# Kernel optimization log

Measured on AMD Instinct MI355X. Metric: run time of the kernel, lower is better.

Reference implementation:

```python
import jax, jax.numpy as jnp
import numpy as np

N_NODES = 50000
N_EDGES = 800000
IN_DIM = 128
HID = 128
NUM_LAYERS = 3
LN_EPS = 1e-5


def setup_inputs() -> dict:
    key = jax.random.key(0)
    ks = jax.random.split(key, 4 + 4 * NUM_LAYERS)
    x = jax.random.normal(ks[0], (N_NODES, IN_DIM), dtype=jnp.float32)
    edge_index = jax.random.randint(ks[1], (2, N_EDGES), 0, N_NODES, dtype=jnp.int32)
    Ws, bs, gammas, betas = [], [], [], []
    d_in = IN_DIM
    for l in range(NUM_LAYERS):
        scale = 1.0 / np.sqrt(d_in)
        Ws.append(jax.random.uniform(ks[2 + 4 * l], (d_in, HID), jnp.float32, -scale, scale))
        bs.append(jnp.zeros((HID,), jnp.float32))
        gammas.append(jnp.ones((HID,), jnp.float32))
        betas.append(jnp.zeros((HID,), jnp.float32))
        d_in = HID
    return {"x": x, "edge_index": edge_index, "Ws": Ws, "bs": bs,
            "gammas": gammas, "betas": betas}


def _gcn_conv(x, src, dst, dinv, norm_e, W, b):
    # GCNConv: h = x W; out = D^{-1/2}(A+I)D^{-1/2} h + b (self loops added)
    h = x @ W                                        # [N, H]
    msg = h[src] * norm_e[:, None]                   # [E, H] gather
    agg = jax.ops.segment_sum(msg, dst, num_segments=N_NODES)  # scatter
    agg = agg + h * (dinv * dinv)[:, None]           # self-loop contribution
    return agg + b


def _layernorm(x, gamma, beta):
    mu = jnp.mean(x, axis=-1, keepdims=True)
    var = jnp.mean(jnp.square(x - mu), axis=-1, keepdims=True)
    return (x - mu) * jax.lax.rsqrt(var + LN_EPS) * gamma + beta


def reference(x, edge_index, Ws, bs, gammas, betas):
    src, dst = edge_index[0], edge_index[1]
    # degree with self loops (PyG: counts on target index, +1 for self loop)
    deg = jax.ops.segment_sum(jnp.ones((N_EDGES,), x.dtype), dst,
                              num_segments=N_NODES) + 1.0
    dinv = jax.lax.rsqrt(deg)                        # deg >= 1 always
    norm_e = dinv[src] * dinv[dst]                   # [E]
    emb = x
    for i in range(NUM_LAYERS):
        h = _gcn_conv(x, src, dst, dinv, norm_e, Ws[i], bs[i])
        emb = h
        x = jax.nn.relu(h)
        # dropout is identity in eval mode
        if i != NUM_LAYERS - 1:
            x = _layernorm(x, gammas[i], betas[i])
    return emb, x
```

## Files before the change

### kernel.cpp

```cpp
#include <hip/hip_runtime.h>
#include <cstddef>

#define HID 128
#define LN_EPS 1e-5f
#define GROWS 8
#define WTP 144

typedef unsigned int uint32;
typedef __attribute__((ext_vector_type(8))) short short8;
typedef __attribute__((ext_vector_type(4))) float f32x4;

__device__ __forceinline__ float wave_sum(float v) {
#pragma unroll
  for (int o = 32; o > 0; o >>= 1) v += __shfl_xor(v, o, 64);
  return v;
}

__device__ __forceinline__ uint32 bf16_rne(float x) {
  uint32 u = __float_as_uint(x);
  u += 0x7fffu + ((u >> 16) & 1u);
  return u >> 16;
}

__device__ __forceinline__ uint32 pack_bf2(float x, float y) {
  uint32 ux = __float_as_uint(x);
  uint32 uy = __float_as_uint(y);
  ux += 0x7fffu + ((ux >> 16) & 1u);
  uy += 0x7fffu + ((uy >> 16) & 1u);
  return (ux >> 16) | (uy & 0xffff0000u);
}

extern "C" __global__ void k_zero(int* __restrict__ p, int n) {
  int i = blockIdx.x * blockDim.x + threadIdx.x;
  if (i < n) p[i] = 0;
}

extern "C" __global__ void k_deg(const int* __restrict__ dst, int* __restrict__ deg, int E) {
  int i = blockIdx.x * blockDim.x + threadIdx.x;
  if (i < E) atomicAdd(&deg[dst[i]], 1);
}

extern "C" __global__ void k_dinv(const int* __restrict__ deg, float* __restrict__ dinv, int N) {
  int i = blockIdx.x * blockDim.x + threadIdx.x;
  if (i < N) dinv[i] = rsqrtf((float)deg[i] + 1.0f);
}

extern "C" __global__ void k_scan1(const int* __restrict__ in, int* __restrict__ exc,
                                   int* __restrict__ bsum, int n) {
  __shared__ int sh[256];
  int tid = threadIdx.x;
  int i = blockIdx.x * 256 + tid;
  int v = (i < n) ? in[i] : 0;
  sh[tid] = v;
  __syncthreads();
  for (int o = 1; o < 256; o <<= 1) {
    int t = (tid >= o) ? sh[tid - o] : 0;
    __syncthreads();
    sh[tid] += t;
    __syncthreads();
  }
  if (i < n) exc[i] = sh[tid] - v;
  if (tid == 255) bsum[blockIdx.x] = sh[255];
}

extern "C" __global__ void k_scan2(const int* __restrict__ bsum, int* __restrict__ bbase, int nb) {
  __shared__ int sh[256];
  int tid = threadIdx.x;
  int v = (tid < nb) ? bsum[tid] : 0;
  sh[tid] = v;
  __syncthreads();
  for (int o = 1; o < 256; o <<= 1) {
    int t = (tid >= o) ? sh[tid - o] : 0;
    __syncthreads();
    sh[tid] += t;
    __syncthreads();
  }
  if (tid < nb) bbase[tid] = sh[tid] - v;
}

extern "C" __global__ void k_scan3(const int* __restrict__ exc, const int* __restrict__ bbase,
                                   const int* __restrict__ deg, int* __restrict__ roff,
                                   int* __restrict__ cursor, float* __restrict__ dinv,
                                   int N, int E) {
  int i = blockIdx.x * blockDim.x + threadIdx.x;
  if (i < N) {
    int o = exc[i] + bbase[i >> 8];
    roff[i] = o;
    cursor[i] = o;
    dinv[i] = rsqrtf((float)deg[i] + 1.0f);
  } else if (i == N) {
    roff[N] = E;
  }
}

extern "C" __global__ void k_fill_p(const int* __restrict__ src, const int* __restrict__ dst,
                                    int* __restrict__ cursor, int* __restrict__ csrc,
                                    int E, int N) {
  int part = blockIdx.x & 7;
  int grp = blockIdx.x >> 3;
  int ngrp = gridDim.x >> 3;
  int lo = (int)((long long)N * part >> 3);
  int hi = (int)((long long)N * (part + 1) >> 3);
  for (int i = grp * blockDim.x + threadIdx.x; i < E; i += ngrp * blockDim.x) {
    int d = dst[i];
    if (d >= lo && d < hi) {
      int pos = atomicAdd(&cursor[d], 1);
      csrc[pos] = src[i];
    }
  }
}

extern "C" __global__ void k_wt3(const float* __restrict__ W0, const float* __restrict__ W1,
                                 const float* __restrict__ W2, unsigned short* __restrict__ wt) {
  int i = blockIdx.x * 256 + threadIdx.x;
  if (i < 3 * HID * HID) {
    int l = i >> 14, r = i & 16383;
    int n = r >> 7, k = r & 127;
    const float* W = (l == 0) ? W0 : ((l == 1) ? W1 : W2);
    wt[i] = (unsigned short)bf16_rne(W[k * HID + n]);
  }
}

template <bool BF>
__global__ __launch_bounds__(256) void k_gemm_t(
    const void* __restrict__ xin, const unsigned short* __restrict__ wt,
    const float* __restrict__ dinv, uint32* __restrict__ gb, int N) {
  __shared__ unsigned short Wt[HID * WTP];
  __shared__ float dv_s[64];
  int tid = threadIdx.x, lane = tid & 63, wv = tid >> 6;
  int r0 = blockIdx.x * 64;
  int nr = min(64, N - r0);
  for (int i = tid; i < 2048; i += 256) {
    short8 v = *(const short8*)(wt + i * 8);
    int n = i >> 4, k0 = (i & 15) * 8;
    *(short8*)&Wt[n * WTP + k0] = v;
  }
  if (tid < 64) dv_s[tid] = (tid < nr) ? dinv[r0 + min(tid, nr - 1)] : 0.f;
  int arow = r0 + wv * 16 + (lane & 15);
  int arow_c = min(arow, N - 1);
  int kb = (lane >> 4) * 8;
  short8 a[4];
  if (BF) {
    const uint32* x32 = (const uint32*)xin;
    const uint32* rp = x32 + (size_t)arow_c * 64 + (kb >> 1);
#pragma unroll
    for (int q = 0; q < 4; ++q) a[q] = *(const short8*)(rp + q * 16);
  } else {
    const float* xf = (const float*)xin;
    const float* rp = xf + (size_t)arow_c * HID + kb;
#pragma unroll
    for (int q = 0; q < 4; ++q) {
      float4 f0 = *(const float4*)(rp + q * 32);
      float4 f1 = *(const float4*)(rp + q * 32 + 4);
      short8 t;
      t[0] = (short)bf16_rne(f0.x);
      t[1] = (short)bf16_rne(f0.y);
      t[2] = (short)bf16_rne(f0.z);
      t[3] = (short)bf16_rne(f0.w);
      t[4] = (short)bf16_rne(f1.x);
      t[5] = (short)bf16_rne(f1.y);
      t[6] = (short)bf16_rne(f1.z);
      t[7] = (short)bf16_rne(f1.w);
      a[q] = t;
    }
  }
  __syncthreads();
  int bn = lane & 15;
#pragma unroll
  for (int c = 0; c < 8; ++c) {
    const unsigned short* wr = &Wt[(c * 16 + bn) * WTP + kb];
    f32x4 acc = {0.f, 0.f, 0.f, 0.f};
    short8 b0 = *(const short8*)(wr + 0);
    short8 b1 = *(const short8*)(wr + 32);
    short8 b2 = *(const short8*)(wr + 64);
    short8 b3 = *(const short8*)(wr + 96);
    acc = __builtin_amdgcn_mfma_f32_16x16x32_bf16(a[0], b0, acc, 0, 0, 0);
    acc = __builtin_amdgcn_mfma_f32_16x16x32_bf16(a[1], b1, acc, 0, 0, 0);
    acc = __builtin_amdgcn_mfma_f32_16x16x32_bf16(a[2], b2, acc, 0, 0, 0);
    acc = __builtin_amdgcn_mfma_f32_16x16x32_bf16(a[3], b3, acc, 0, 0, 0);
#pragma unroll
    for (int reg = 0; reg < 4; ++reg) {
      float v = acc[reg];
      float p = __shfl_xor(v, 1, 64);
      int row = wv * 16 + (lane >> 4) * 4 + reg;
      if (!(lane & 1) && row < nr) {
        float dvv = dv_s[row];
        gb[(size_t)(r0 + row) * 64 + (c * 8 + (bn >> 1))] = pack_bf2(v * dvv, p * dvv);
      }
    }
  }
}

extern "C" __global__ __launch_bounds__(256) void k_agg_bf(
    const uint32* __restrict__ gb, const int* __restrict__ roff, const int* __restrict__ csrc,
    const float* __restrict__ dinv, const float* __restrict__ bias,
    const float* __restrict__ gamma, const float* __restrict__ beta,
    uint32* __restrict__ out_bf, float* __restrict__ out0, float* __restrict__ out1,
    int N, int mode) {
  int w = (int)((blockIdx.x * blockDim.x + threadIdx.x) >> 6);
  int lane = threadIdx.x & 63;
  if (w >= N) return;
  uint32 us = gb[(size_t)w * 64 + lane];
  int e = roff[w], e1 = roff[w + 1];
  float ax = __uint_as_float(us << 16);
  float ay = __uint_as_float(us & 0xffff0000u);
  for (; e + 8 <= e1; e += 8) {
#pragma unroll
    for (int i = 0; i < 8; ++i) {
      int s = csrc[e + i];
      uint32 u = gb[(size_t)s * 64 + lane];
      ax += __uint_as_float(u << 16);
      ay += __uint_as_float(u & 0xffff0000u);
    }
  }
  if (e < e1) {
#pragma unroll
    for (int i = 0; i < 8; ++i) {
      int idx = e + i;
      int cl = (idx < e1) ? idx : (e1 - 1);
      int s = csrc[cl];
      uint32 u = gb[(size_t)s * 64 + lane];
      float m = (idx < e1) ? 1.f : 0.f;
      ax = fmaf(m, __uint_as_float(u << 16), ax);
      ay = fmaf(m, __uint_as_float(u & 0xffff0000u), ay);
    }
  }
  float dv = dinv[w];
  float2 bb = *(const float2*)(bias + 2 * lane);
  float hx = fmaf(ax, dv, bb.x);
  float hy = fmaf(ay, dv, bb.y);
  if (mode) {
    *(float2*)(out0 + (size_t)w * HID + 2 * lane) = make_float2(hx, hy);
    *(float2*)(out1 + (size_t)w * HID + 2 * lane) =
        make_float2(fmaxf(hx, 0.f), fmaxf(hy, 0.f));
  } else {
    float rx = fmaxf(hx, 0.f), ry = fmaxf(hy, 0.f);
    float mu = wave_sum(rx + ry) * (1.f / HID);
    float dx = rx - mu, dy = ry - mu;
    float var = wave_sum(dx * dx + dy * dy) * (1.f / HID);
    float sc = rsqrtf(var + LN_EPS);
    float2 ga = *(const float2*)(gamma + 2 * lane);
    float2 be = *(const float2*)(beta + 2 * lane);
    out_bf[(size_t)w * 64 + lane] =
        pack_bf2(fmaf(dx * sc, ga.x, be.x), fmaf(dy * sc, ga.y, be.y));
  }
}

extern "C" __global__ __launch_bounds__(256) void k_gemm(
    const float* __restrict__ x, const float* __restrict__ W,
    const float* __restrict__ dinv, float* __restrict__ g, int N) {
  __shared__ float Wl[HID * HID];
  __shared__ float xl[4][GROWS * HID];
  int tid = threadIdx.x;
#pragma unroll
  for (int i = 0; i < (HID * HID / 4) / 256; ++i)
    ((float4*)Wl)[tid + 256 * i] = ((const float4*)W)[tid + 256 * i];
  __syncthreads();
  int wid = tid >> 6, lane = tid & 63;
  float* xw = xl[wid];
  int nchunks = (N + GROWS - 1) / GROWS;
  int gw = blockIdx.x * 4 + wid;
  int nw = gridDim.x * 4;
  for (int chunk = gw; chunk < nchunks; chunk += nw) {
    int r0 = chunk * GROWS;
    int nr = min(GROWS, N - r0);
    const float4* xs = (const float4*)(x + (size_t)r0 * HID);
    float4* xd = (float4*)xw;
    if (nr == GROWS) {
#pragma unroll
      for (int i = 0; i < 4; ++i) xd[lane + 64 * i] = xs[lane + 64 * i];
    } else {
      for (int i = lane; i < nr * (HID / 4); i += 64) xd[i] = xs[i];
    }
    float2 acc[GROWS];
#pragma unroll
    for (int r = 0; r < GROWS; ++r) acc[r] = make_float2(0.f, 0.f);
    for (int k = 0; k < HID; k += 4) {
      float2 w0 = *(const float2*)&Wl[(k + 0) * HID + 2 * lane];
      float2 w1 = *(const float2*)&Wl[(k + 1) * HID + 2 * lane];
      float2 w2 = *(const float2*)&Wl[(k + 2) * HID + 2 * lane];
      float2 w3 = *(const float2*)&Wl[(k + 3) * HID + 2 * lane];
#pragma unroll
      for (int r = 0; r < GROWS; ++r) {
        float4 xq = *(const float4*)&xw[r * HID + k];
        acc[r].x = fmaf(xq.w, w3.x, fmaf(xq.z, w2.x, fmaf(xq.y, w1.x, fmaf(xq.x, w0.x, acc[r].x))));
        acc[r].y = fmaf(xq.w, w3.y, fmaf(xq.z, w2.y, fmaf(xq.y, w1.y, fmaf(xq.x, w0.y, acc[r].y))));
      }
    }
#pragma unroll
    for (int r = 0; r < GROWS; ++r) {
      if (r < nr) {
        float dv = dinv[r0 + r];
        *(float2*)(g + (size_t)(r0 + r) * HID + 2 * lane) =
            make_float2(acc[r].x * dv, acc[r].y * dv);
      }
    }
  }
}

extern "C" __global__ void k_copy(const float* __restrict__ in, float* __restrict__ out, int n4) {
  int i = blockIdx.x * blockDim.x + threadIdx.x;
  if (i < n4) ((float4*)out)[i] = ((const float4*)in)[i];
}

extern "C" __global__ void k_scatter(const float* __restrict__ g, const int* __restrict__ src,
                                     const int* __restrict__ dst, float* __restrict__ acc, int E) {
  int e = (int)((blockIdx.x * blockDim.x + threadIdx.x) >> 6);
  int lane = threadIdx.x & 63;
  if (e >= E) return;
  int s = src[e], d = dst[e];
  float2 v = *(const float2*)(g + (size_t)s * HID + 2 * lane);
  float* p = acc + (size_t)d * HID + 2 * lane;
  atomicAdd(p, v.x);
  atomicAdd(p + 1, v.y);
}

extern "C" __global__ __launch_bounds__(256) void k_fin(
    float* __restrict__ a, const float* __restrict__ dinv, const float* __restrict__ bias,
    const float* __restrict__ gamma, const float* __restrict__ beta, int N, int last) {
  int w = (int)((blockIdx.x * blockDim.x + threadIdx.x) >> 6);
  int lane = threadIdx.x & 63;
  if (w >= N) return;
  float2 acc = *(const float2*)(a + (size_t)w * HID + 2 * lane);
  float dv = dinv[w];
  float2 bb = *(const float2*)(bias + 2 * lane);
  float hx = fmaf(acc.x, dv, bb.x);
  float hy = fmaf(acc.y, dv, bb.y);
  if (last) {
    *(float2*)(a + (size_t)w * HID + 2 * lane) = make_float2(hx, hy);
  } else {
    float rx = fmaxf(hx, 0.f), ry = fmaxf(hy, 0.f);
    float mu = wave_sum(rx + ry) * (1.f / HID);
    float dx = rx - mu, dy = ry - mu;
    float var = wave_sum(dx * dx + dy * dy) * (1.f / HID);
    float sc = rsqrtf(var + LN_EPS);
    float2 ga = *(const float2*)(gamma + 2 * lane);
    float2 be = *(const float2*)(beta + 2 * lane);
    *(float2*)(a + (size_t)w * HID + 2 * lane) =
        make_float2(fmaf(dx * sc, ga.x, be.x), fmaf(dy * sc, ga.y, be.y));
  }
}

extern "C" __global__ void k_relu(const float* __restrict__ in, float* __restrict__ out, int n4) {
  int i = blockIdx.x * blockDim.x + threadIdx.x;
  if (i < n4) {
    float4 v = ((const float4*)in)[i];
    v.x = fmaxf(v.x, 0.f);
    v.y = fmaxf(v.y, 0.f);
    v.z = fmaxf(v.z, 0.f);
    v.w = fmaxf(v.w, 0.f);
    ((float4*)out)[i] = v;
  }
}

extern "C" void kernel_launch(void* const* d_in, const int* in_sizes, int n_in,
                              void* d_out, int out_size, void* d_ws, size_t ws_size,
                              hipStream_t stream) {
  const float* x0 = (const float*)d_in[0];
  const int* ei = (const int*)d_in[1];
  int N = in_sizes[0] / HID;
  int E = in_sizes[1] / 2;

  const float* W[3];
  const float* b[3];
  const float* gm[3];
  const float* bt[3];
  if (n_in >= 14 && in_sizes[2] == HID * HID) {
    for (int l = 0; l < 3; ++l) {
      W[l] = (const float*)d_in[2 + l];
      b[l] = (const float*)d_in[5 + l];
      gm[l] = (const float*)d_in[8 + l];
      bt[l] = (const float*)d_in[11 + l];
    }
  } else if (n_in >= 6) {
    const float* Wc = (const float*)d_in[2];
    const float* bc = (const float*)d_in[3];
    const float* gc = (const float*)d_in[4];
    const float* tc = (const float*)d_in[5];
    for (int l = 0; l < 3; ++l) {
      W[l] = Wc + (size_t)l * HID * HID;
      b[l] = bc + (size_t)l * HID;
      gm[l] = gc + (size_t)l * HID;
      bt[l] = tc + (size_t)l * HID;
    }
  } else {
    return;
  }
  const int* src = ei;
  const int* dst = ei + E;

  float* OUT0 = (float*)d_out;
  float* OUT1 = OUT0 + (size_t)N * HID;

  auto align256 = [](size_t bytes) { return (bytes + 255) & ~(size_t)255; };
  size_t o_dinv = 0;
  size_t o_roff = o_dinv + align256((size_t)N * 4);
  size_t o_csrc = o_roff + align256((size_t)(N + 1) * 4);
  size_t o_wt3 = o_csrc + align256((size_t)E * 4);
  size_t o_gbf = o_wt3 + align256((size_t)3 * HID * HID * 2);
  size_t o_act = o_gbf + align256((size_t)N * 256);
  size_t need_full = o_act + (size_t)N * 256;
  size_t need_scatter = align256((size_t)N * 4);
  if (ws_size < need_scatter) return;

  char* wp = (char*)d_ws;
  float* dinv = (float*)(wp + o_dinv);

  int n4 = N * HID / 4;
  int aggBlocks = (N * 64 + 255) / 256;

  if (ws_size >= need_full) {
    int* roff = (int*)(wp + o_roff);
    int* csrc = (int*)(wp + o_csrc);
    unsigned short* wt3 = (unsigned short*)(wp + o_wt3);
    uint32* gbf = (uint32*)(wp + o_gbf);
    uint32* act = (uint32*)(wp + o_act);

    int* deg = (int*)OUT1;
    int* exc = deg + N;
    int* cursor = exc + N;
    int* bsum = cursor + N;
    int* bbase = bsum + 256;

    k_zero<<<(N + 255) / 256, 256, 0, stream>>>(deg, N);
    k_deg<<<(E + 255) / 256, 256, 0, stream>>>(dst, deg, E);
    int nb = (N + 255) / 256;
    k_scan1<<<nb, 256, 0, stream>>>(deg, exc, bsum, N);
    k_scan2<<<1, 256, 0, stream>>>(bsum, bbase, nb);
    k_scan3<<<(N + 256) / 256, 256, 0, stream>>>(exc, bbase, deg, roff, cursor, dinv, N, E);
    k_fill_p<<<2048, 256, 0, stream>>>(src, dst, cursor, csrc, E, N);
    k_wt3<<<(3 * HID * HID + 255) / 256, 256, 0, stream>>>(W[0], W[1], W[2], wt3);

    int gemmBlocks = (N + 63) / 64;
    k_gemm_t<false><<<gemmBlocks, 256, 0, stream>>>(x0, wt3, dinv, gbf, N);
    k_agg_bf<<<aggBlocks, 256, 0, stream>>>(gbf, roff, csrc, dinv, b[0], gm[0], bt[0],
                                            act, nullptr, nullptr, N, 0);
    k_gemm_t<true><<<gemmBlocks, 256, 0, stream>>>(act, wt3 + HID * HID, dinv, gbf, N);
    k_agg_bf<<<aggBlocks, 256, 0, stream>>>(gbf, roff, csrc, dinv, b[1], gm[1], bt[1],
                                            act, nullptr, nullptr, N, 0);
    k_gemm_t<true><<<gemmBlocks, 256, 0, stream>>>(act, wt3 + 2 * HID * HID, dinv, gbf, N);
    k_agg_bf<<<aggBlocks, 256, 0, stream>>>(gbf, roff, csrc, dinv, b[2], gm[2], bt[2],
                                            nullptr, OUT0, OUT1, N, 3);
  } else {
    int* deg = (int*)OUT1;
    k_zero<<<(N + 255) / 256, 256, 0, stream>>>(deg, N);
    k_deg<<<(E + 255) / 256, 256, 0, stream>>>(dst, deg, E);
    k_dinv<<<(N + 255) / 256, 256, 0, stream>>>(deg, dinv, N);
    int scatBlocks = (E * 64 + 255) / 256;
    for (int l = 0; l < 3; ++l) {
      const float* xin = (l == 0) ? x0 : OUT0;
      int last = (l == 2);
      k_gemm<<<512, 256, 0, stream>>>(xin, W[l], dinv, OUT1, N);
      k_copy<<<(n4 + 255) / 256, 256, 0, stream>>>(OUT1, OUT0, n4);
      k_scatter<<<scatBlocks, 256, 0, stream>>>(OUT1, src, dst, OUT0, E);
      k_fin<<<aggBlocks, 256, 0, stream>>>(OUT0, dinv, b[l], gm[l], bt[l], N, last);
    }
    k_relu<<<(n4 + 255) / 256, 256, 0, stream>>>(OUT0, OUT1, n4);
  }
}
```

Measured before the change: 235.0 us.

## Gather four edges per wave with 16-byte loads in aggregation; fuse setup kernels

The aggregation kernel now splits each wave into four 16-lane groups. Each group handles a different neighbor edge and loads a full 256-byte bf16 row as uint4 per lane, and the partial sums are then reduced across groups with shuffles. The intent is fewer, wider memory transactions and more gathers in flight per wave, at the cost of more registers and extra shuffles. Separately, the degree-zeroing and weight-transpose kernels are merged into one launch to save a kernel launch.

```diff
diff --git a/kernel.cpp b/kernel.cpp
--- a/kernel.cpp
+++ b/kernel.cpp
@@ -30,9 +30,22 @@
   return (ux >> 16) | (uy & 0xffff0000u);
 }
 
-extern "C" __global__ void k_zero(int* __restrict__ p, int n) {
-  int i = blockIdx.x * blockDim.x + threadIdx.x;
-  if (i < n) p[i] = 0;
+extern "C" __global__ void k_setup(int* __restrict__ deg, int N, int zb,
+                                   const float* __restrict__ W0, const float* __restrict__ W1,
+                                   const float* __restrict__ W2, unsigned short* __restrict__ wt) {
+  int bx = blockIdx.x;
+  if (bx < zb) {
+    int i = bx * 256 + threadIdx.x;
+    if (i < N) deg[i] = 0;
+  } else {
+    int i = (bx - zb) * 256 + threadIdx.x;
+    if (i < 3 * HID * HID) {
+      int l = i >> 14, r = i & 16383;
+      int n = r >> 7, k = r & 127;
+      const float* W = (l == 0) ? W0 : ((l == 1) ? W1 : W2);
+      wt[i] = (unsigned short)bf16_rne(W[k * HID + n]);
+    }
+  }
 }
 
 extern "C" __global__ void k_deg(const int* __restrict__ dst, int* __restrict__ deg, int E) {
@@ -110,17 +123,6 @@
   }
 }
 
-extern "C" __global__ void k_wt3(const float* __restrict__ W0, const float* __restrict__ W1,
-                                 const float* __restrict__ W2, unsigned short* __restrict__ wt) {
-  int i = blockIdx.x * 256 + threadIdx.x;
-  if (i < 3 * HID * HID) {
-    int l = i >> 14, r = i & 16383;
-    int n = r >> 7, k = r & 127;
-    const float* W = (l == 0) ? W0 : ((l == 1) ? W1 : W2);
-    wt[i] = (unsigned short)bf16_rne(W[k * HID + n]);
-  }
-}
-
 template <bool BF>
 __global__ __launch_bounds__(256) void k_gemm_t(
     const void* __restrict__ xin, const unsigned short* __restrict__ wt,
@@ -200,49 +202,99 @@
   int w = (int)((blockIdx.x * blockDim.x + threadIdx.x) >> 6);
   int lane = threadIdx.x & 63;
   if (w >= N) return;
-  uint32 us = gb[(size_t)w * 64 + lane];
+  int g = lane >> 4, c = lane & 15;
+  float acc[8];
+  {
+    uint4 u = ((const uint4*)(gb + (size_t)w * 64))[c];
+    float m = (g == 0) ? 1.f : 0.f;
+    acc[0] = m * __uint_as_float(u.x << 16);
+    acc[1] = m * __uint_as_float(u.x & 0xffff0000u);
+    acc[2] = m * __uint_as_float(u.y << 16);
+    acc[3] = m * __uint_as_float(u.y & 0xffff0000u);
+    acc[4] = m * __uint_as_float(u.z << 16);
+    acc[5] = m * __uint_as_float(u.z & 0xffff0000u);
+    acc[6] = m * __uint_as_float(u.w << 16);
+    acc[7] = m * __uint_as_float(u.w & 0xffff0000u);
+  }
   int e = roff[w], e1 = roff[w + 1];
-  float ax = __uint_as_float(us << 16);
-  float ay = __uint_as_float(us & 0xffff0000u);
-  for (; e + 8 <= e1; e += 8) {
+  for (; e + 4 <= e1; e += 4) {
+    int s = csrc[e + g];
+    uint4 u = ((const uint4*)(gb + (size_t)s * 64))[c];
+    acc[0] += __uint_as_float(u.x << 16);
+    acc[1] += __uint_as_float(u.x & 0xffff0000u);
+    acc[2] += __uint_as_float(u.y << 16);
+    acc[3] += __uint_as_float(u.y & 0xffff0000u);
+    acc[4] += __uint_as_float(u.z << 16);
+    acc[5] += __uint_as_float(u.z & 0xffff0000u);
+    acc[6] += __uint_as_float(u.w << 16);
+    acc[7] += __uint_as_float(u.w & 0xffff0000u);
+  }
+  if (g < e1 - e) {
+    int s = csrc[e + g];
+    uint4 u = ((const uint4*)(gb + (size_t)s * 64))[c];
+    acc[0] += __uint_as_float(u.x << 16);
+    acc[1] += __uint_as_float(u.x & 0xffff0000u);
+    acc[2] += __uint_as_float(u.y << 16);
+    acc[3] += __uint_as_float(u.y & 0xffff0000u);
+    acc[4] += __uint_as_float(u.z << 16);
+    acc[5] += __uint_as_float(u.z & 0xffff0000u);
+    acc[6] += __uint_as_float(u.w << 16);
+    acc[7] += __uint_as_float(u.w & 0xffff0000u);
+  }
+#pragma unroll
+  for (int i = 0; i < 8; ++i) {
+    acc[i] += __shfl_xor(acc[i], 16, 64);
+    acc[i] += __shfl_xor(acc[i], 32, 64);
+  }
+  float dv = dinv[w];
+  float4 bb0 = *(const float4*)(bias + c * 8);
+  float4 bb1 = *(const float4*)(bias + c * 8 + 4);
+  float h[8];
+  h[0] = fmaf(acc[0], dv, bb0.x);
+  h[1] = fmaf(acc[1], dv, bb0.y);
+  h[2] = fmaf(acc[2], dv, bb0.z);
+  h[3] = fmaf(acc[3], dv, bb0.w);
+  h[4] = fmaf(acc[4], dv, bb1.x);
+  h[5] = fmaf(acc[5], dv, bb1.y);
+  h[6] = fmaf(acc[6], dv, bb1.z);
+  h[7] = fmaf(acc[7], dv, bb1.w);
+  if (mode) {
+    if (g == 0) {
+      float4* o0 = (float4*)(out0 + (size_t)w * HID + c * 8);
+      o0[0] = make_float4(h[0], h[1], h[2], h[3]);
+      o0[1] = make_float4(h[4], h[5], h[6], h[7]);
+      float4* o1 = (float4*)(out1 + (size_t)w * HID + c * 8);
+      o1[0] = make_float4(fmaxf(h[0], 0.f), fmaxf(h[1], 0.f), fmaxf(h[2], 0.f), fmaxf(h[3], 0.f));
+      o1[1] = make_float4(fmaxf(h[4], 0.f), fmaxf(h[5], 0.f), fmaxf(h[6], 0.f), fmaxf(h[7], 0.f));
+    }
+  } else {
+    float r[8], s8 = 0.f;
 #pragma unroll
     for (int i = 0; i < 8; ++i) {
-      int s = csrc[e + i];
-      uint32 u = gb[(size_t)s * 64 + lane];
-      ax += __uint_as_float(u << 16);
-      ay += __uint_as_float(u & 0xffff0000u);
-    }
-  }
-  if (e < e1) {
+      r[i] = fmaxf(h[i], 0.f);
+      s8 += r[i];
+    }
+    float mu = wave_sum(s8) * (1.f / (HID * 4));
+    float vs = 0.f;
 #pragma unroll
     for (int i = 0; i < 8; ++i) {
-      int idx = e + i;
-      int cl = (idx < e1) ? idx : (e1 - 1);
-      int s = csrc[cl];
-      uint32 u = gb[(size_t)s * 64 + lane];
-      float m = (idx < e1) ? 1.f : 0.f;
-      ax = fmaf(m, __uint_as_float(u << 16), ax);
-      ay = fmaf(m, __uint_as_float(u & 0xffff0000u), ay);
-    }
-  }
-  float dv = dinv[w];
-  float2 bb = *(const float2*)(bias + 2 * lane);
-  float hx = fmaf(ax, dv, bb.x);
-  float hy = fmaf(ay, dv, bb.y);
-  if (mode) {
-    *(float2*)(out0 + (size_t)w * HID + 2 * lane) = make_float2(hx, hy);
-    *(float2*)(out1 + (size_t)w * HID + 2 * lane) =
-        make_float2(fmaxf(hx, 0.f), fmaxf(hy, 0.f));
-  } else {
-    float rx = fmaxf(hx, 0.f), ry = fmaxf(hy, 0.f);
-    float mu = wave_sum(rx + ry) * (1.f / HID);
-    float dx = rx - mu, dy = ry - mu;
-    float var = wave_sum(dx * dx + dy * dy) * (1.f / HID);
+      r[i] -= mu;
+      vs = fmaf(r[i], r[i], vs);
+    }
+    float var = wave_sum(vs) * (1.f / (HID * 4));
     float sc = rsqrtf(var + LN_EPS);
-    float2 ga = *(const float2*)(gamma + 2 * lane);
-    float2 be = *(const float2*)(beta + 2 * lane);
-    out_bf[(size_t)w * 64 + lane] =
-        pack_bf2(fmaf(dx * sc, ga.x, be.x), fmaf(dy * sc, ga.y, be.y));
+    if (g == 0) {
+      float4 ga0 = *(const float4*)(gamma + c * 8);
+      float4 ga1 = *(const float4*)(gamma + c * 8 + 4);
+      float4 be0 = *(const float4*)(beta + c * 8);
+      float4 be1 = *(const float4*)(beta + c * 8 + 4);
+      uint4 o;
+      o.x = pack_bf2(fmaf(r[0] * sc, ga0.x, be0.x), fmaf(r[1] * sc, ga0.y, be0.y));
+      o.y = pack_bf2(fmaf(r[2] * sc, ga0.z, be0.z), fmaf(r[3] * sc, ga0.w, be0.w));
+      o.z = pack_bf2(fmaf(r[4] * sc, ga1.x, be1.x), fmaf(r[5] * sc, ga1.y, be1.y));
+      o.w = pack_bf2(fmaf(r[6] * sc, ga1.z, be1.z), fmaf(r[7] * sc, ga1.w, be1.w));
+      ((uint4*)(out_bf + (size_t)w * 64))[c] = o;
+    }
   }
 }
 
@@ -422,14 +474,15 @@
     int* bsum = cursor + N;
     int* bbase = bsum + 256;
 
-    k_zero<<<(N + 255) / 256, 256, 0, stream>>>(deg, N);
+    int zb = (N + 255) / 256;
+    int wtb = (3 * HID * HID + 255) / 256;
+    k_setup<<<zb + wtb, 256, 0, stream>>>(deg, N, zb, W[0], W[1], W[2], wt3);
     k_deg<<<(E + 255) / 256, 256, 0, stream>>>(dst, deg, E);
     int nb = (N + 255) / 256;
     k_scan1<<<nb, 256, 0, stream>>>(deg, exc, bsum, N);
     k_scan2<<<1, 256, 0, stream>>>(bsum, bbase, nb);
     k_scan3<<<(N + 256) / 256, 256, 0, stream>>>(exc, bbase, deg, roff, cursor, dinv, N, E);
     k_fill_p<<<2048, 256, 0, stream>>>(src, dst, cursor, csrc, E, N);
-    k_wt3<<<(3 * HID * HID + 255) / 256, 256, 0, stream>>>(W[0], W[1], W[2], wt3);
 
     int gemmBlocks = (N + 63) / 64;
     k_gemm_t<false><<<gemmBlocks, 256, 0, stream>>>(x0, wt3, dinv, gbf, N);
@@ -443,7 +496,8 @@
                                             nullptr, OUT0, OUT1, N, 3);
   } else {
     int* deg = (int*)OUT1;
-    k_zero<<<(N + 255) / 256, 256, 0, stream>>>(deg, N);
+    k_setup<<<(N + 255) / 256, 256, 0, stream>>>(deg, N, (N + 255) / 256,
+                                                 W[0], W[1], W[2], nullptr);
     k_deg<<<(E + 255) / 256, 256, 0, stream>>>(dst, deg, E);
     k_dinv<<<(N + 255) / 256, 256, 0, stream>>>(deg, dinv, N);
     int scatBlocks = (E * 64 + 255) / 256;
```

New measurement: 252.6 us. 1.07x slower.
